# Kernel tuning notes

Hardware: AMD Instinct MI355X
Metric: run time of the kernel (lower is better)

The kernel has to match this reference:

```python
import jax, jax.numpy as jnp
import numpy as np

H = 64   # hidden_size
N = 128  # input_size (num nodes)
B = 64   # batch
T = 96   # seq_len
LN_EPS = 1e-5


def setup_inputs() -> dict:
    key = jax.random.key(0)
    ks = jax.random.split(key, 4)
    x = jax.random.normal(ks[0], (B, T, N), jnp.float32)
    # xavier_uniform-like scale for per-node gate weights [N, 1+H, 4H]
    lim = float(np.sqrt(6.0 / ((1 + H) + 4 * H)))
    w = jax.random.uniform(ks[1], (N, 1 + H, 4 * H), jnp.float32, -lim, lim)
    b = jnp.zeros((N, 4 * H), jnp.float32)
    ln_g = jnp.ones((H,), jnp.float32)
    ln_b = jnp.zeros((H,), jnp.float32)
    fc_w = jax.random.normal(ks[2], (1, H), jnp.float32) * (1.0 / np.sqrt(H))
    fc_b = jnp.zeros((1,), jnp.float32)
    return {"x": x, "w": w, "b": b, "ln_g": ln_g, "ln_b": ln_b,
            "fc_w": fc_w, "fc_b": fc_b}


def _crelu(z):
    return jnp.maximum(z.real, 0) + 1j * jnp.maximum(z.imag, 0)


def _csigmoid(z):
    # torch.sigmoid on complex: 1/(1+exp(-z))
    return 1.0 / (1.0 + jnp.exp(-z))


def _fc_att(x, pool_axes):
    # adaptive_avg_pool to 1 over pool_axes, (C)ReLU, sigmoid, rescale
    squeeze = jnp.mean(x, axis=pool_axes, keepdims=True)
    if jnp.iscomplexobj(x):
        exc = _crelu(squeeze)
        return x * _csigmoid(exc)
    exc = jnp.maximum(squeeze, 0)
    return x * jax.nn.sigmoid(exc)


def reference(x, w, b, ln_g, ln_b, fc_w, fc_b):
    Bb, Tt, Nn = x.shape
    h0 = jnp.zeros((Bb, Nn, H), x.dtype)
    c0 = jnp.zeros((Bb, Nn, H), x.dtype)

    def step(carry, x_t):  # x_t: [B, N]
        h, c = carry
        comb = jnp.concatenate([x_t[..., None], h], axis=-1)      # [B,N,1+H]
        gates = jnp.einsum('bni,nio->bno', comb, w) + b            # [B,N,4H]
        i_g, f_g, o_g, c_tilda = jnp.split(gates, 4, axis=-1)
        # NOTE: original cell does NOT apply tanh to c_tilda
        c_new = jax.nn.sigmoid(f_g) * c + jax.nn.sigmoid(i_g) * c_tilda
        h_new = jax.nn.sigmoid(o_g) * jnp.tanh(c_new)
        return (h_new, c_new), h_new

    _, hs = jax.lax.scan(step, (h0, c0), jnp.swapaxes(x, 0, 1))    # [T,B,N,H]
    lstm_out = jnp.sum(hs, axis=0)                                  # sum over time -> [B,N,H]

    # inter_op: FFT pairwise interaction over the node axis
    m = jnp.fft.rfft(lstm_out, axis=1, norm='ortho')                # [B,F,H] complex, F=N//2+1
    x_f = m[:, :, None, :] * m[:, None, :, :]                       # [B,F,F,H]
    x_f = _fc_att(x_f, (2, 3))
    x_f = jnp.sum(x_f, axis=1)                                      # [B,F,H]
    n_out = 2 * (x_f.shape[1] - 1)                                  # torch irfft default n
    feats = jnp.fft.irfft(x_f, n=n_out, axis=1, norm='ortho')       # [B,N,H] real
    feats = _fc_att(feats, (2,))
    out = jnp.sum(feats, axis=1)                                    # [B,H]

    # LayerNorm(H) -> Linear(H,1) -> sigmoid
    mu = jnp.mean(out, axis=-1, keepdims=True)
    var = jnp.var(out, axis=-1, keepdims=True)
    out = (out - mu) / jnp.sqrt(var + LN_EPS) * ln_g + ln_b
    out = out @ fc_w.T + fc_b                                       # [B,1]
    return jax.nn.sigmoid(out)
```

## Files before the change

### kernel.cpp

```cpp
#include <hip/hip_runtime.h>
#include <math.h>

#define T_STEPS 96
#define N_NODES 128
#define B_SZ 64
#define H_SZ 64

typedef __attribute__((ext_vector_type(8))) __bf16 bf16x8;
typedef __attribute__((ext_vector_type(4))) float f32x4;

__device__ __forceinline__ float rcp_fast(float x){ return __builtin_amdgcn_rcpf(x); }
__device__ __forceinline__ float sigm(float v){ return rcp_fast(1.0f + __expf(-v)); }
__device__ __forceinline__ float tanh_fast(float v){
  float e = __expf(2.0f*v);
  return fmaf(-2.0f, rcp_fast(e + 1.0f), 1.0f);
}

__global__ __launch_bounds__(256, 2) void lstm_kernel(
    const float* __restrict__ x, const float* __restrict__ w,
    const float* __restrict__ bias, float* __restrict__ yout)
{
  __shared__ __align__(16) unsigned short hb[2][16*72];
  __shared__ __align__(16) float xsl[T_STEPS*20];

  const int n   = blockIdx.x >> 2;
  const int bq  = blockIdx.x & 3;
  const int tid = threadIdx.x;
  const int wv  = tid >> 6;
  const int ln  = tid & 63;
  const int l15 = ln & 15;
  const int q   = ln >> 4;
  const int hh  = wv*16 + l15;

  for (int i = tid; i < 2*16*72; i += 256) hb[0][i] = 0;
  for (int i = tid; i < T_STEPS*16; i += 256){
    int t2 = i >> 4, bl = i & 15;
    xsl[t2*20 + bl] = x[(bq*16 + bl)*(T_STEPS*N_NODES) + t2*N_NODES + n];
  }

  const float* wn = w + n*(65*256);
  bf16x8 bHi[4][2], bLo[4][2];
  float w0g[4], bg[4];
#pragma unroll
  for (int g = 0; g < 4; ++g){
    const int col = g*64 + hh;
    w0g[g] = wn[col];
    bg[g]  = bias[n*256 + col];
#pragma unroll
    for (int ks = 0; ks < 2; ++ks){
#pragma unroll
      for (int j = 0; j < 8; ++j){
        float wf = wn[(1 + ks*32 + q*8 + j)*256 + col];
        __bf16 hi = (__bf16)wf;
        __bf16 lo = (__bf16)(wf - (float)hi);
        bHi[g][ks][j] = hi;
        bLo[g][ks][j] = lo;
      }
    }
  }

  f32x4 cv  = {0.f,0.f,0.f,0.f};
  f32x4 hsv = {0.f,0.f,0.f,0.f};
  __syncthreads();

#pragma unroll 2
  for (int t = 0; t < T_STEPS; ++t){
    const unsigned short* cur = hb[t & 1];
    unsigned short*       nxt = hb[(t & 1) ^ 1];

    bf16x8 a0 = *(const bf16x8*)&cur[l15*72 +  0 + q*8];
    bf16x8 a1 = *(const bf16x8*)&cur[l15*72 + 32 + q*8];
    f32x4 xv = *(const f32x4*)&xsl[t*20 + q*4];

    f32x4 acc[4];
#pragma unroll
    for (int g = 0; g < 4; ++g){
      f32x4 a = xv * w0g[g] + bg[g];
      a = __builtin_amdgcn_mfma_f32_16x16x32_bf16(a0, bHi[g][0], a, 0,0,0);
      a = __builtin_amdgcn_mfma_f32_16x16x32_bf16(a0, bLo[g][0], a, 0,0,0);
      a = __builtin_amdgcn_mfma_f32_16x16x32_bf16(a1, bHi[g][1], a, 0,0,0);
      a = __builtin_amdgcn_mfma_f32_16x16x32_bf16(a1, bLo[g][1], a, 0,0,0);
      acc[g] = a;
    }

    f32x4 sI, sF, sO;
#pragma unroll
    for (int r = 0; r < 4; ++r){
      sI[r] = sigm(acc[0][r]);
      sF[r] = sigm(acc[1][r]);
      sO[r] = sigm(acc[2][r]);
    }
    cv = sF*cv + sI*acc[3];
    f32x4 th;
#pragma unroll
    for (int r = 0; r < 4; ++r) th[r] = tanh_fast(cv[r]);
    f32x4 hn = sO*th;
    hsv += hn;
#pragma unroll
    for (int r = 0; r < 4; ++r){
      __bf16 hv = (__bf16)hn[r];
      nxt[(q*4+r)*72 + hh] = __builtin_bit_cast(unsigned short, hv);
    }
    __syncthreads();
  }

#pragma unroll
  for (int r = 0; r < 4; ++r){
    const int b = bq*16 + q*4 + r;
    yout[(b*N_NODES + n)*H_SZ + hh] = hsv[r];
  }
}

__global__ __launch_bounds__(256, 2) void dft_kernel(
    const float* __restrict__ y, float* __restrict__ Mout)
{
  __shared__ __align__(16) float ysl[128*20];
  __shared__ float twc[128], tws[128];
  const int b   = blockIdx.x >> 2;
  const int hg  = blockIdx.x & 3;
  const int tid = threadIdx.x;

  if (tid < 128){
    float ang = (float)((double)tid * 0.04908738521234052);
    twc[tid] = cosf(ang);
    tws[tid] = sinf(ang);
  }
  for (int i = tid; i < 128*16; i += 256){
    int nn = i >> 4, h = i & 15;
    ysl[nn*20 + h] = y[(b*N_NODES + nn)*H_SZ + hg*16 + h];
  }
  __syncthreads();

  for (int o = tid; o < 65*4; o += 256){
    int k  = o >> 2;
    int hq = o & 3;
    float re0=0,re1=0,re2=0,re3=0,im0=0,im1=0,im2=0,im3=0;
    for (int nn = 0; nn < 128; ++nn){
      float4 yv = *(const float4*)&ysl[nn*20 + hq*4];
      int j = (k*nn) & 127;
      float cc = twc[j], ss = tws[j];
      re0 = fmaf(yv.x, cc, re0); im0 = fmaf(yv.x, -ss, im0);
      re1 = fmaf(yv.y, cc, re1); im1 = fmaf(yv.y, -ss, im1);
      re2 = fmaf(yv.z, cc, re2); im2 = fmaf(yv.z, -ss, im2);
      re3 = fmaf(yv.w, cc, re3); im3 = fmaf(yv.w, -ss, im3);
    }
    const float s = 0.08838834764831845f;
    const int hb2 = hg*16 + hq*4;
    float* mre = Mout + ((b*2+0)*65 + k)*H_SZ + hb2;
    float* mim = Mout + ((b*2+1)*65 + k)*H_SZ + hb2;
    mre[0]=re0*s; mre[1]=re1*s; mre[2]=re2*s; mre[3]=re3*s;
    mim[0]=im0*s; mim[1]=im1*s; mim[2]=im2*s; mim[3]=im3*s;
  }
}

__global__ __launch_bounds__(256, 1) void post_kernel(
    const float* __restrict__ y, const float* __restrict__ Mws,
    const float* __restrict__ ln_g, const float* __restrict__ ln_b,
    const float* __restrict__ fc_w, const float* __restrict__ fc_b,
    float* __restrict__ out)
{
  __shared__ float ysh[128*65];
  __shared__ float Mre[65*65];
  __shared__ float Mim[65*65];
  __shared__ float twc[128], tws[128];
  __shared__ float Sre[64], Sim[64];
  __shared__ float gr[65], gi[65];
  __shared__ float Gre[64], Gim[64];
  __shared__ float att[128];
  __shared__ float PQ[65*2], AA[65*2];
  __shared__ float outv[64];

  const int b   = blockIdx.x;
  const int tid = threadIdx.x;

  if (tid < 128){
    float ang = (float)((double)tid * 0.04908738521234052);
    twc[tid] = cosf(ang);
    tws[tid] = sinf(ang);
  }
  for (int i = tid; i < 128*16; i += 256){
    int nn = i >> 4, h4 = (i & 15)*4;
    float4 v = *(const float4*)&y[(b*N_NODES + nn)*H_SZ + h4];
    ysh[nn*65 + h4+0] = v.x; ysh[nn*65 + h4+1] = v.y;
    ysh[nn*65 + h4+2] = v.z; ysh[nn*65 + h4+3] = v.w;
  }
  for (int i = tid; i < 65*16; i += 256){
    int k = i >> 4, h4 = (i & 15)*4;
    float4 vr = *(const float4*)&Mws[((b*2+0)*65 + k)*H_SZ + h4];
    float4 vi = *(const float4*)&Mws[((b*2+1)*65 + k)*H_SZ + h4];
    Mre[k*65 + h4+0] = vr.x; Mre[k*65 + h4+1] = vr.y;
    Mre[k*65 + h4+2] = vr.z; Mre[k*65 + h4+3] = vr.w;
    Mim[k*65 + h4+0] = vi.x; Mim[k*65 + h4+1] = vi.y;
    Mim[k*65 + h4+2] = vi.z; Mim[k*65 + h4+3] = vi.w;
  }
  __syncthreads();

  if (tid < 64){
    float sr=0, si=0;
    for (int k = 0; k < 65; ++k){ sr += Mre[k*65+tid]; si += Mim[k*65+tid]; }
    Sre[tid]=sr; Sim[tid]=si;
  }
  __syncthreads();

  if (tid < 65){
    float a=0, bb=0;
    for (int h = 0; h < 64; ++h){
      float mr = Mre[tid*65+h], mi = Mim[tid*65+h];
      a  += mr*Sre[h] - mi*Sim[h];
      bb += mr*Sim[h] + mi*Sre[h];
    }
    a  *= (1.0f/4160.0f);  bb *= (1.0f/4160.0f);
    a = fmaxf(a, 0.0f);    bb = fmaxf(bb, 0.0f);
    float t  = __expf(-a);
    float cb = cosf(bb), sb = sinf(bb);
    float dre = 1.0f + t*cb;
    float dim = t*sb;
    float nrm = rcp_fast(dre*dre + dim*dim);
    gr[tid] = dre*nrm;
    gi[tid] = dim*nrm;
  }
  __syncthreads();

  if (tid < 64){
    float grh=0, gih=0;
    for (int k = 0; k < 65; ++k){
      float mr = Mre[k*65+tid], mi = Mim[k*65+tid];
      float gk = gr[k], hk = gi[k];
      grh += gk*mr - hk*mi;
      gih += gk*mi + hk*mr;
    }
    Gre[tid]=grh; Gim[tid]=gih;
  }
  __syncthreads();

  if (tid < 65){
    float p=0, qq=0;
    for (int h = 0; h < 64; ++h){
      float gimh = Gim[h];
      p  += gimh * Mim[tid*65+h];
      qq += gimh * Mre[tid*65+h];
    }
    const float s2 = 2.0f*0.08838834764831845f;
    PQ[tid*2]   = p*s2;
    PQ[tid*2+1] = qq*s2;
  }
  __syncthreads();

  if (tid < 128){
    float u=0;
    for (int h = 0; h < 64; ++h) u += Gre[h]*ysh[tid*65+h];
    float v=0;
    for (int k = 1; k < 64; ++k){
      int j = (k*tid) & 127;
      v += PQ[k*2]*twc[j] + PQ[k*2+1]*tws[j];
    }
    float mean = (u - v)*(1.0f/64.0f);
    att[tid] = sigm(fmaxf(mean, 0.0f));
  }
  __syncthreads();

  if (tid < 65){
    float ac=0, as=0;
    for (int nn = 0; nn < 128; ++nn){
      int j = (tid*nn) & 127;
      float a2 = att[nn];
      ac = fmaf(a2, twc[j], ac);
      as = fmaf(a2, tws[j], as);
    }
    const float s2 = 2.0f*0.08838834764831845f;
    AA[tid*2]   = ac*s2;
    AA[tid*2+1] = as*s2;
  }
  __syncthreads();

  if (tid < 64){
    float wyh=0;
    for (int nn = 0; nn < 128; ++nn) wyh += att[nn]*ysh[nn*65+tid];
    float wHh=0;
    for (int k = 1; k < 64; ++k)
      wHh += Mim[k*65+tid]*AA[k*2] + Mre[k*65+tid]*AA[k*2+1];
    outv[tid] = Gre[tid]*wyh - Gim[tid]*wHh;
  }
  __syncthreads();

  if (tid < 64){
    float o = outv[tid];
    float s = o;
    for (int off = 32; off; off >>= 1) s += __shfl_xor(s, off, 64);
    float mu = s*(1.0f/64.0f);
    float d  = o - mu;
    float vv = d*d;
    for (int off = 32; off; off >>= 1) vv += __shfl_xor(vv, off, 64);
    float var = vv*(1.0f/64.0f);
    float zo = (d / sqrtf(var + 1e-5f))*ln_g[tid] + ln_b[tid];
    float z  = zo * fc_w[tid];
    for (int off = 32; off; off >>= 1) z += __shfl_xor(z, off, 64);
    if (tid == 0) out[b] = 1.0f/(1.0f + __expf(-(z + fc_b[0])));
  }
}

extern "C" void kernel_launch(void* const* d_in, const int* in_sizes, int n_in,
                              void* d_out, int out_size, void* d_ws, size_t ws_size,
                              hipStream_t stream) {
  (void)in_sizes; (void)n_in; (void)out_size; (void)ws_size;
  const float* x    = (const float*)d_in[0];
  const float* w    = (const float*)d_in[1];
  const float* bia  = (const float*)d_in[2];
  const float* ln_g = (const float*)d_in[3];
  const float* ln_b = (const float*)d_in[4];
  const float* fc_w = (const float*)d_in[5];
  const float* fc_b = (const float*)d_in[6];
  float* out = (float*)d_out;

  float* y = (float*)d_ws;
  float* M = y + (size_t)B_SZ*N_NODES*H_SZ;

  lstm_kernel<<<dim3(512), dim3(256), 0, stream>>>(x, w, bia, y);
  dft_kernel <<<dim3(256), dim3(256), 0, stream>>>(y, M);
  post_kernel<<<dim3(64),  dim3(256), 0, stream>>>(y, M, ln_g, ln_b, fc_w, fc_b, out);
}
```

Before: 181.5 us.

## Drop bf16 hi/lo split, transpose MFMA operands, fold log2e into weights

The LSTM recurrence now uses a single bf16 copy of the weights instead of a hi+lo split pair, which halves the MFMAs per gate per step. It also swaps the MFMA operand roles so each lane owns four contiguous hidden units, allowing packed 8-byte LDS stores of h and float4 output stores. log2(e) is pre-folded into the gate weights and bias, so the activations use raw exp2. The cost is reduced weight precision in the recurrence, which may increase error accumulated over the 96 steps.

```diff
diff --git a/kernel.cpp b/kernel.cpp
--- a/kernel.cpp
+++ b/kernel.cpp
@@ -10,18 +10,15 @@
 typedef __attribute__((ext_vector_type(4))) float f32x4;
 
 __device__ __forceinline__ float rcp_fast(float x){ return __builtin_amdgcn_rcpf(x); }
+__device__ __forceinline__ float exp2_fast(float x){ return __builtin_amdgcn_exp2f(x); }
 __device__ __forceinline__ float sigm(float v){ return rcp_fast(1.0f + __expf(-v)); }
-__device__ __forceinline__ float tanh_fast(float v){
-  float e = __expf(2.0f*v);
-  return fmaf(-2.0f, rcp_fast(e + 1.0f), 1.0f);
-}
 
 __global__ __launch_bounds__(256, 2) void lstm_kernel(
     const float* __restrict__ x, const float* __restrict__ w,
     const float* __restrict__ bias, float* __restrict__ yout)
 {
   __shared__ __align__(16) unsigned short hb[2][16*72];
-  __shared__ __align__(16) float xsl[T_STEPS*20];
+  __shared__ float xsl[T_STEPS*16];
 
   const int n   = blockIdx.x >> 2;
   const int bq  = blockIdx.x & 3;
@@ -30,32 +27,32 @@
   const int ln  = tid & 63;
   const int l15 = ln & 15;
   const int q   = ln >> 4;
-  const int hh  = wv*16 + l15;
-
-  for (int i = tid; i < 2*16*72; i += 256) hb[0][i] = 0;
+
+  for (int i = tid; i < 2*16*72; i += 256) ((unsigned short*)hb)[i] = 0;
   for (int i = tid; i < T_STEPS*16; i += 256){
     int t2 = i >> 4, bl = i & 15;
-    xsl[t2*20 + bl] = x[(bq*16 + bl)*(T_STEPS*N_NODES) + t2*N_NODES + n];
-  }
-
+    xsl[i] = x[(bq*16 + bl)*(T_STEPS*N_NODES) + t2*N_NODES + n];
+  }
+
+  const float LOG2E = 1.4426950408889634f;
   const float* wn = w + n*(65*256);
-  bf16x8 bHi[4][2], bLo[4][2];
-  float w0g[4], bg[4];
+
+  bf16x8 aF[4][2];
+  f32x4 w04[4], bg4[4];
 #pragma unroll
   for (int g = 0; g < 4; ++g){
-    const int col = g*64 + hh;
-    w0g[g] = wn[col];
-    bg[g]  = bias[n*256 + col];
-#pragma unroll
-    for (int ks = 0; ks < 2; ++ks){
-#pragma unroll
-      for (int j = 0; j < 8; ++j){
-        float wf = wn[(1 + ks*32 + q*8 + j)*256 + col];
-        __bf16 hi = (__bf16)wf;
-        __bf16 lo = (__bf16)(wf - (float)hi);
-        bHi[g][ks][j] = hi;
-        bLo[g][ks][j] = lo;
-      }
+    const float sc = (g < 3) ? LOG2E : 1.0f;
+    const int colA = g*64 + wv*16 + l15;
+#pragma unroll
+    for (int ks = 0; ks < 2; ++ks)
+#pragma unroll
+      for (int j = 0; j < 8; ++j)
+        aF[g][ks][j] = (__bf16)(wn[(1 + ks*32 + q*8 + j)*256 + colA] * sc);
+#pragma unroll
+    for (int r = 0; r < 4; ++r){
+      const int colD = g*64 + wv*16 + q*4 + r;
+      w04[g][r] = wn[colD] * sc;
+      bg4[g][r] = bias[n*256 + colD] * sc;
     }
   }
 
@@ -66,49 +63,48 @@
 #pragma unroll 2
   for (int t = 0; t < T_STEPS; ++t){
     const unsigned short* cur = hb[t & 1];
-    unsigned short*       nxt = hb[(t & 1) ^ 1];
-
-    bf16x8 a0 = *(const bf16x8*)&cur[l15*72 +  0 + q*8];
-    bf16x8 a1 = *(const bf16x8*)&cur[l15*72 + 32 + q*8];
-    f32x4 xv = *(const f32x4*)&xsl[t*20 + q*4];
+    unsigned short*       nxt = (unsigned short*)hb[(t & 1) ^ 1];
+
+    bf16x8 b0 = *(const bf16x8*)&cur[l15*72 +  0 + q*8];
+    bf16x8 b1 = *(const bf16x8*)&cur[l15*72 + 32 + q*8];
+    float xv = xsl[t*16 + l15];
 
     f32x4 acc[4];
 #pragma unroll
     for (int g = 0; g < 4; ++g){
-      f32x4 a = xv * w0g[g] + bg[g];
-      a = __builtin_amdgcn_mfma_f32_16x16x32_bf16(a0, bHi[g][0], a, 0,0,0);
-      a = __builtin_amdgcn_mfma_f32_16x16x32_bf16(a0, bLo[g][0], a, 0,0,0);
-      a = __builtin_amdgcn_mfma_f32_16x16x32_bf16(a1, bHi[g][1], a, 0,0,0);
-      a = __builtin_amdgcn_mfma_f32_16x16x32_bf16(a1, bLo[g][1], a, 0,0,0);
+      f32x4 a = w04[g]*xv + bg4[g];
+      a = __builtin_amdgcn_mfma_f32_16x16x32_bf16(aF[g][0], b0, a, 0,0,0);
+      a = __builtin_amdgcn_mfma_f32_16x16x32_bf16(aF[g][1], b1, a, 0,0,0);
       acc[g] = a;
     }
 
-    f32x4 sI, sF, sO;
+    f32x4 sI, sF, sO, th;
 #pragma unroll
     for (int r = 0; r < 4; ++r){
-      sI[r] = sigm(acc[0][r]);
-      sF[r] = sigm(acc[1][r]);
-      sO[r] = sigm(acc[2][r]);
+      sI[r] = rcp_fast(1.0f + exp2_fast(-acc[0][r]));
+      sF[r] = rcp_fast(1.0f + exp2_fast(-acc[1][r]));
+      sO[r] = rcp_fast(1.0f + exp2_fast(-acc[2][r]));
     }
     cv = sF*cv + sI*acc[3];
-    f32x4 th;
-#pragma unroll
-    for (int r = 0; r < 4; ++r) th[r] = tanh_fast(cv[r]);
+#pragma unroll
+    for (int r = 0; r < 4; ++r){
+      float e = exp2_fast(cv[r]*2.8853900817779268f);
+      th[r] = fmaf(-2.0f, rcp_fast(e + 1.0f), 1.0f);
+    }
     f32x4 hn = sO*th;
     hsv += hn;
-#pragma unroll
-    for (int r = 0; r < 4; ++r){
-      __bf16 hv = (__bf16)hn[r];
-      nxt[(q*4+r)*72 + hh] = __builtin_bit_cast(unsigned short, hv);
-    }
+
+    ushort4 pk;
+    pk.x = __builtin_bit_cast(unsigned short, (__bf16)hn[0]);
+    pk.y = __builtin_bit_cast(unsigned short, (__bf16)hn[1]);
+    pk.z = __builtin_bit_cast(unsigned short, (__bf16)hn[2]);
+    pk.w = __builtin_bit_cast(unsigned short, (__bf16)hn[3]);
+    *(ushort4*)&nxt[l15*72 + wv*16 + q*4] = pk;
     __syncthreads();
   }
 
-#pragma unroll
-  for (int r = 0; r < 4; ++r){
-    const int b = bq*16 + q*4 + r;
-    yout[(b*N_NODES + n)*H_SZ + hh] = hsv[r];
-  }
+  float4 o4 = {hsv[0], hsv[1], hsv[2], hsv[3]};
+  *(float4*)&yout[((bq*16 + l15)*N_NODES + n)*H_SZ + wv*16 + q*4] = o4;
 }
 
 __global__ __launch_bounds__(256, 2) void dft_kernel(
```

Result: faster. 165.6 us (-8.8%).
